# Kernel tuning notes

Measured on AMD Instinct MI355X. Metric: run time of the kernel, lower is better.

The kernel has to match this reference:

```python
import jax, jax.numpy as jnp
import numpy as np

# Model dims (match init_kwargs)
D_MODEL = 2048
H = 16        # query heads
HKV = 4       # kv heads (GQA)
DS = 32       # semantic head dim (compressed)
DG = 32       # geometric head dim (compressed, RoPE'd)
DV = 64       # value head dim
B, T = 2, 4096
MB = 64       # mem_block
LW = 1024     # local_window
ROPE_BASE = 10000.0
NEG_INF = -1e9


def _rope(x, pos, base):
    # x: [B, h, T, d] with d even; standard rotate-half RoPE
    d = x.shape[-1]
    inv_freq = 1.0 / (base ** (jnp.arange(0, d, 2, dtype=jnp.float32) / d))
    ang = pos.astype(jnp.float32)[:, None] * inv_freq          # [T, d/2]
    cos, sin = jnp.cos(ang), jnp.sin(ang)                      # [T, d/2]
    x1, x2 = jnp.split(x, 2, axis=-1)
    return jnp.concatenate([x1 * cos - x2 * sin,
                            x2 * cos + x1 * sin], axis=-1)


def setup_inputs() -> dict:
    key = jax.random.key(0)
    ks = jax.random.split(key, 8)
    w = lambda k, sh: jax.random.normal(k, sh, jnp.float32) * 0.02
    return {
        "x": jax.random.normal(ks[0], (B, T, D_MODEL), jnp.float32),
        "Wq_sem": w(ks[1], (D_MODEL, H * DS)),
        "Wk_sem": w(ks[2], (D_MODEL, HKV * DS)),
        "Wq_geo": w(ks[3], (D_MODEL, H * DG)),
        "Wk_geo": w(ks[4], (D_MODEL, HKV * DG)),
        "Wv": w(ks[5], (D_MODEL, HKV * DV)),
        "Wo": w(ks[6], (H * DV, D_MODEL)),
        "logit_scale": jnp.zeros((H,), jnp.float32),
    }


def reference(x, Wq_sem, Wk_sem, Wq_geo, Wk_geo, Wv, Wo, logit_scale):
    Bq, Tq = x.shape[0], x.shape[1]
    split = lambda y, h, d: y.reshape(Bq, Tq, h, d).transpose(0, 2, 1, 3)
    # Decoupled projections
    q_sem = split(x @ Wq_sem, H, DS)      # [B,H,T,DS]
    k_sem = split(x @ Wk_sem, HKV, DS)    # [B,HKV,T,DS]
    q_geo = split(x @ Wq_geo, H, DG)
    k_geo = split(x @ Wk_geo, HKV, DG)
    v = split(x @ Wv, HKV, DV)            # [B,HKV,T,DV]
    pos = jnp.arange(Tq)
    # RoPE only on the geometric path
    q_geo = _rope(q_geo, pos, ROPE_BASE)
    k_geo = _rope(k_geo, pos, ROPE_BASE)
    # Memory-block summarization: mean-pool remote KV into one token per block
    remote = Tq - LW
    nblk = remote // MB
    pool = lambda a: jnp.concatenate(
        [a[:, :, :remote].reshape(Bq, HKV, nblk, MB, a.shape[-1]).mean(axis=3),
         a[:, :, remote:]], axis=2)
    k_sem2, k_geo2, v2 = pool(k_sem), pool(k_geo), pool(v)  # [B,HKV,K,*], K=nblk+LW
    k_pos = jnp.concatenate([jnp.arange(nblk) * MB + (MB - 1),
                             jnp.arange(remote, Tq)])        # [K]
    # GQA head-group broadcast
    rep = lambda a: jnp.repeat(a, H // HKV, axis=1)
    k_sem2, k_geo2, v2 = rep(k_sem2), rep(k_geo2), rep(v2)   # [B,H,K,*]
    # Decoupled scores: semantic + geometric, each with its own scale
    scores = (jnp.einsum('bhqd,bhkd->bhqk', q_sem, k_sem2) * (1.0 / jnp.sqrt(float(DS)))
              + jnp.einsum('bhqd,bhkd->bhqk', q_geo, k_geo2) * (1.0 / jnp.sqrt(float(DG))))
    # Learned per-head temperature
    scores = scores * jnp.exp(logit_scale)[None, :, None, None]
    # Causal mask over summarized key positions
    mask = k_pos[None, :] <= pos[:, None]                    # [T,K]
    scores = jnp.where(mask[None, None], scores, NEG_INF)
    probs = jax.nn.softmax(scores, axis=-1)
    out = jnp.einsum('bhqk,bhkd->bhqd', probs, v2)           # [B,H,T,DV]
    out = out.transpose(0, 2, 1, 3).reshape(Bq, Tq, H * DV)
    return out @ Wo                                          # [B,T,D_MODEL]
```

## Files before the change

kernel.cpp:

```cpp
#include <hip/hip_runtime.h>
#include <math.h>

#define B_  2
#define T_  4096
#define DM  2048
#define H_  16
#define HKV 4
#define DV_ 64
#define MB_ 64
#define LW_ 1024
#define REMOTE 3072
#define NBLK 48
#define KTOT 1072
#define NTILES 17

typedef __bf16 bf16x8 __attribute__((ext_vector_type(8)));
typedef float  f32x4  __attribute__((ext_vector_type(4)));

__device__ __forceinline__ float bf2f(unsigned short u) {
    unsigned int x = ((unsigned int)u) << 16;
    return __builtin_bit_cast(float, x);
}
__device__ __forceinline__ unsigned short f2bf(float f) {
    unsigned int x = __builtin_bit_cast(unsigned int, f);
    x = x + 0x7fffu + ((x >> 16) & 1u);
    return (unsigned short)(x >> 16);
}

__device__ __forceinline__ void gload16(const void* gsrc, unsigned short* ldst) {
    __builtin_amdgcn_global_load_lds(
        (const __attribute__((address_space(1))) void*)gsrc,
        (__attribute__((address_space(3))) void*)ldst,
        16, 0, 0);
}

__global__ void transpose_all(const float* __restrict__ Wq_sem,
                              const float* __restrict__ Wq_geo,
                              const float* __restrict__ Wk_sem,
                              const float* __restrict__ Wk_geo,
                              const float* __restrict__ Wv,
                              const float* __restrict__ Wo,
                              unsigned short* __restrict__ WcatT,
                              unsigned short* __restrict__ WoT) {
    __shared__ float tile[32][33];
    const int bid = blockIdx.x;
    const float* src; unsigned short* dst; int R, C, tiles_x, lt;
    if (bid < 1024)      { src = Wq_sem; dst = WcatT;                       R = 2048; C = 512;  tiles_x = 16; lt = bid; }
    else if (bid < 2048) { src = Wq_geo; dst = WcatT + (size_t)512  * 2048; R = 2048; C = 512;  tiles_x = 16; lt = bid - 1024; }
    else if (bid < 2304) { src = Wk_sem; dst = WcatT + (size_t)1024 * 2048; R = 2048; C = 128;  tiles_x = 4;  lt = bid - 2048; }
    else if (bid < 2560) { src = Wk_geo; dst = WcatT + (size_t)1152 * 2048; R = 2048; C = 128;  tiles_x = 4;  lt = bid - 2304; }
    else if (bid < 3072) { src = Wv;     dst = WcatT + (size_t)1280 * 2048; R = 2048; C = 256;  tiles_x = 8;  lt = bid - 2560; }
    else                 { src = Wo;     dst = WoT;                         R = 1024; C = 2048; tiles_x = 64; lt = bid - 3072; }
    const int ct = lt % tiles_x, rt = lt / tiles_x;
    const int tx = threadIdx.x, ty = threadIdx.y;
    #pragma unroll
    for (int i = ty; i < 32; i += 8)
        tile[i][tx] = src[(size_t)(rt * 32 + i) * C + ct * 32 + tx];
    __syncthreads();
    #pragma unroll
    for (int i = ty; i < 32; i += 8)
        dst[(size_t)(ct * 32 + i) * R + rt * 32 + tx] = f2bf(tile[tx][i]);
}

__global__ __launch_bounds__(256, 3) void gemmProj(
    const float* __restrict__ Axf0,
    const unsigned short* __restrict__ BT,
    unsigned short* __restrict__ qcat,
    unsigned short* __restrict__ kp,
    unsigned short* __restrict__ vt,
    int K, int nbx)
{
    extern __shared__ __align__(16) unsigned short lds[];

    const int tid = threadIdx.x;
    const int lane = tid & 63, w = tid >> 6;
    const int wr = w >> 1, wc = w & 1;
    const int l15 = lane & 15, lg = lane >> 4;

    const int cpx = gridDim.x >> 3;
    const int swz = (blockIdx.x & 7) * cpx + (blockIdx.x >> 3);
    const int bx = swz % nbx, by = swz / nbx;
    const int row0 = by * 128, col0 = bx * 128;

    const int scol = ((lane & 3) ^ ((lane >> 3) & 3)) * 8;
    const int srA = w * 16 + (lane >> 2);
    const unsigned short* Bg = BT + (size_t)col0 * K;

    const int ar0 = tid >> 2, ar1 = ar0 + 64, ac = tid & 3;
    const int agc0 = (ac ^ ((ar0 >> 1) & 3)) * 8;
    const int agc1 = (ac ^ ((ar1 >> 1) & 3)) * 8;
    const float* Axf = Axf0 + (size_t)row0 * K;

    const int rdsw = (lg ^ ((l15 >> 1) & 3)) * 8;
    const int aoff = (wr * 64 + l15) * 32 + rdsw;
    const int boff = (wc * 64 + l15) * 32 + rdsw;

    const int NT = K >> 5;
    f32x4 acc[4][4] = {};

    auto stageB = [&](int s, int kk) {
        unsigned short* sb = lds + s * 8192 + 4096;
        #pragma unroll
        for (int j = 0; j < 2; j++)
            gload16(Bg + (size_t)(srA + j * 64) * K + kk + scol,
                    sb + (j * 256 + w * 64) * 8);
    };
    auto issueA = [&](float4* ra, int kk) {
        ra[0] = *(const float4*)&Axf[(size_t)ar0 * K + kk + agc0];
        ra[1] = *(const float4*)&Axf[(size_t)ar0 * K + kk + agc0 + 4];
        ra[2] = *(const float4*)&Axf[(size_t)ar1 * K + kk + agc1];
        ra[3] = *(const float4*)&Axf[(size_t)ar1 * K + kk + agc1 + 4];
    };
    auto writeA = [&](int s, const float4* ra) {
        unsigned short* sa = lds + s * 8192;
        bf16x8 v0, v1;
        v0[0] = (__bf16)ra[0].x; v0[1] = (__bf16)ra[0].y;
        v0[2] = (__bf16)ra[0].z; v0[3] = (__bf16)ra[0].w;
        v0[4] = (__bf16)ra[1].x; v0[5] = (__bf16)ra[1].y;
        v0[6] = (__bf16)ra[1].z; v0[7] = (__bf16)ra[1].w;
        v1[0] = (__bf16)ra[2].x; v1[1] = (__bf16)ra[2].y;
        v1[2] = (__bf16)ra[2].z; v1[3] = (__bf16)ra[2].w;
        v1[4] = (__bf16)ra[3].x; v1[5] = (__bf16)ra[3].y;
        v1[6] = (__bf16)ra[3].z; v1[7] = (__bf16)ra[3].w;
        *(uint4*)&sa[ar0 * 32 + ac * 8] = __builtin_bit_cast(uint4, v0);
        *(uint4*)&sa[ar1 * 32 + ac * 8] = __builtin_bit_cast(uint4, v1);
    };
    auto mfmaTile = [&](int rs_) {
        const unsigned short* As_ = lds + rs_ * 8192;
        const unsigned short* Bs_ = As_ + 4096;
        bf16x8 af[4], bfr[4];
        #pragma unroll
        for (int mf = 0; mf < 4; mf++)
            af[mf] = __builtin_bit_cast(bf16x8, *(const uint4*)&As_[aoff + mf * 512]);
        #pragma unroll
        for (int nf = 0; nf < 4; nf++)
            bfr[nf] = __builtin_bit_cast(bf16x8, *(const uint4*)&Bs_[boff + nf * 512]);
        __builtin_amdgcn_s_setprio(1);
        #pragma unroll
        for (int mf = 0; mf < 4; mf++)
            #pragma unroll
            for (int nf = 0; nf < 4; nf++)
                acc[mf][nf] = __builtin_amdgcn_mfma_f32_16x16x32_bf16(
                    af[mf], bfr[nf], acc[mf][nf], 0, 0, 0);
        __builtin_amdgcn_s_setprio(0);
    };

    stageB(0, 0);
    stageB(1, 32);
    __builtin_amdgcn_sched_barrier(0);
    float4 rA[4], rB[4];
    issueA(rA, 0);
    issueA(rB, 32);
    writeA(0, rA);
    asm volatile("s_waitcnt lgkmcnt(0)" ::: "memory");
    __builtin_amdgcn_s_barrier();

    int rs = 0;
    for (int t = 0; t < NT; t += 2) {
        const int s1 = (rs == 2) ? 0 : rs + 1;
        const int s2 = (s1 == 2) ? 0 : s1 + 1;
        if (t + 2 < NT) {
            stageB(s2, (t + 2) << 5);
            __builtin_amdgcn_sched_barrier(0);
            issueA(rA, (t + 2) << 5);
        }
        writeA(s1, rB);
        mfmaTile(rs);
        asm volatile("s_waitcnt lgkmcnt(0)" ::: "memory");
        __builtin_amdgcn_s_barrier();
        if (t + 3 < NT) {
            stageB(rs, (t + 3) << 5);
            __builtin_amdgcn_sched_barrier(0);
            issueA(rB, (t + 3) << 5);
        }
        if (t + 2 < NT) writeA(s2, rA);
        mfmaTile(s1);
        asm volatile("s_waitcnt lgkmcnt(0)" ::: "memory");
        __builtin_amdgcn_s_barrier();
        rs = s2;
    }

    const int cspan = col0 + wc * 64;
    const int tbase = row0 & 4095;
    const int bq = row0 >> 12;

    if ((cspan >= 512 && cspan < 1024) || (cspan >= 1152 && cspan < 1280)) {
        const float invf = exp2f(-(float)l15 * 0.8304820237218406f);
        #pragma unroll
        for (int mf = 0; mf < 4; mf++) {
            #pragma unroll
            for (int r = 0; r < 4; r++) {
                float s, c;
                sincosf((float)(tbase + wr*64 + mf*16 + lg*4 + r) * invf, &s, &c);
                float a0 = acc[mf][0][r], a1 = acc[mf][1][r];
                acc[mf][0][r] = a0 * c - a1 * s;
                acc[mf][1][r] = a1 * c + a0 * s;
                float a2 = acc[mf][2][r], a3 = acc[mf][3][r];
                acc[mf][2][r] = a2 * c - a3 * s;
                acc[mf][3][r] = a3 * c + a2 * s;
            }
        }
    }

    if (cspan < 1024) {
        #pragma unroll
        for (int nf = 0; nf < 4; nf++) {
            int col = cspan + nf * 16 + l15;
            int h = (col < 512) ? (col >> 5) : ((col - 512) >> 5);
            int d = (col < 512) ? (col & 31) : (32 + (col & 31));
            unsigned short* qb =
                qcat + (((size_t)(bq * 16 + h)) * 4096 + tbase) * 64 + d;
            #pragma unroll
            for (int mf = 0; mf < 4; mf++)
                #pragma unroll
                for (int r = 0; r < 4; r++)
                    qb[(size_t)(wr*64 + mf*16 + lg*4 + r) * 64] =
                        f2bf(acc[mf][nf][r]);
        }
    } else if (tbase >= REMOTE) {
        #pragma unroll
        for (int nf = 0; nf < 4; nf++) {
            int col = cspan + nf * 16 + l15;
            #pragma unroll
            for (int mf = 0; mf < 4; mf++)
                #pragma unroll
                for (int r = 0; r < 4; r++) {
                    int key = tbase + wr*64 + mf*16 + lg*4 + r - 3024;
                    unsigned short hv = f2bf(acc[mf][nf][r]);
                    if (col < 1280) {
                        int g, dk;
                        if (col < 1152) { g = (col - 1024) >> 5; dk = col & 31; }
                        else            { g = (col - 1152) >> 5; dk = 32 + (col & 31); }
                        kp[(((size_t)(bq*4 + g)) * KTOT + key) * 64 + dk] = hv;
                    } else {
                        int g = (col - 1280) >> 6, dv = col & 63;
                        vt[(((size_t)(bq*4 + g)) * 64 + dv) * KTOT + key] = hv;
                    }
                }
        }
    } else {
        #pragma unroll
        for (int nf = 0; nf < 4; nf++) {
            float ps = 0.f;
            #pragma unroll
            for (int mf = 0; mf < 4; mf++)
                #pragma unroll
                for (int r = 0; r < 4; r++) ps += acc[mf][nf][r];
            ps += __shfl_xor(ps, 16);
            ps += __shfl_xor(ps, 32);
            if (lane < 16) {
                int col = cspan + nf * 16 + l15;
                int key = (tbase >> 6) + wr;
                unsigned short hv = f2bf(ps * (1.f / 64.f));
                if (col < 1280) {
                    int g, dk;
                    if (col < 1152) { g = (col - 1024) >> 5; dk = col & 31; }
                    else            { g = (col - 1152) >> 5; dk = 32 + (col & 31); }
                    kp[(((size_t)(bq*4 + g)) * KTOT + key) * 64 + dk] = hv;
                } else {
                    int g = (col - 1280) >> 6, dv = col & 63;
                    vt[(((size_t)(bq*4 + g)) * 64 + dv) * KTOT + key] = hv;
                }
            }
        }
    }
}

__global__ __launch_bounds__(256, 2) void gemmWo(
    const unsigned short* __restrict__ A,
    const unsigned short* __restrict__ BT,
    float* __restrict__ outF,
    int N, int K, int nbx)
{
    extern __shared__ __align__(16) unsigned short lds[];

    const int tid = threadIdx.x;
    const int lane = tid & 63, w = tid >> 6;
    const int l15 = lane & 15, lg = lane >> 4;

    const int cpx = gridDim.x >> 3;
    const int swz = (blockIdx.x & 7) * cpx + (blockIdx.x >> 3);
    const int bx = swz % nbx, by = swz / nbx;
    const int row0 = by * 128, col0 = bx * 256;

    const int scol = ((lane & 3) ^ ((lane >> 3) & 3)) * 8;
    const int srA = w * 16 + (lane >> 2);
    const unsigned short* Ag = A  + (size_t)row0 * K;
    const unsigned short* Bg = BT + (size_t)col0 * K;

    const int rdsw = (lg ^ ((l15 >> 1) & 3)) * 8;
    const int aoff = l15 * 32 + rdsw;
    const int boff = (w * 64 + l15) * 32 + rdsw;

    const int NT = K >> 5;
    f32x4 acc[8][4] = {};

    auto stage = [&](int s, int kk) {
        unsigned short* sa = lds + s * 12288;
        unsigned short* sb = sa + 4096;
        #pragma unroll
        for (int j = 0; j < 2; j++)
            gload16(Ag + (size_t)(srA + j * 64) * K + kk + scol,
                    sa + (j * 256 + w * 64) * 8);
        #pragma unroll
        for (int j = 0; j < 4; j++)
            gload16(Bg + (size_t)(srA + j * 64) * K + kk + scol,
                    sb + (j * 256 + w * 64) * 8);
    };

    stage(0, 0);
    stage(1, 32);
    asm volatile("s_waitcnt vmcnt(6)" ::: "memory");

    int rs = 0;
    for (int t = 0; t < NT; ++t) {
        __builtin_amdgcn_s_barrier();
        if (t + 2 < NT) stage(rs == 0 ? 2 : rs - 1, (t + 2) << 5);

        const unsigned short* As_ = lds + rs * 12288;
        const unsigned short* Bs_ = As_ + 4096;
        bf16x8 af[8], bfr[4];
        #pragma unroll
        for (int mf = 0; mf < 8; mf++)
            af[mf] = __builtin_bit_cast(bf16x8, *(const uint4*)&As_[aoff + mf * 512]);
        #pragma unroll
        for (int nf = 0; nf < 4; nf++)
            bfr[nf] = __builtin_bit_cast(bf16x8, *(const uint4*)&Bs_[boff + nf * 512]);

        __builtin_amdgcn_s_setprio(1);
        #pragma unroll
        for (int mf = 0; mf < 8; mf++)
            #pragma unroll
            for (int nf = 0; nf < 4; nf++)
                acc[mf][nf] = __builtin_amdgcn_mfma_f32_16x16x32_bf16(
                                  af[mf], bfr[nf], acc[mf][nf], 0, 0, 0);
        __builtin_amdgcn_s_setprio(0);

        if (t + 2 < NT) asm volatile("s_waitcnt vmcnt(6)" ::: "memory");
        else            asm volatile("s_waitcnt vmcnt(0)" ::: "memory");
        rs = (rs == 2) ? 0 : rs + 1;
    }

    #pragma unroll
    for (int mf = 0; mf < 8; mf++)
        #pragma unroll
        for (int nf = 0; nf < 4; nf++)
            #pragma unroll
            for (int r = 0; r < 4; r++) {
                int row = row0 + mf * 16 + lg * 4 + r;
                int col = col0 + w * 64 + nf * 16 + l15;
                outF[(size_t)row * N + col] = acc[mf][nf][r];
            }
}

__global__ __launch_bounds__(256) void attn_fwd(
    const unsigned short* __restrict__ qcat,
    const unsigned short* __restrict__ kp,
    const unsigned short* __restrict__ vt,
    const float* __restrict__ ls,
    unsigned short* __restrict__ attn_out)
{
    __shared__ unsigned short Pl[4][32][72];

    const int tid = threadIdx.x;
    const int lane = tid & 63, w = tid >> 6;
    const int l15 = lane & 15, lg = lane >> 4;

    const int wid = blockIdx.x * 4 + w;
    const int hb = wid & 31;
    const int iu = wid >> 5;
    int i;
    if (iu < 32)       i = 127 - iu;
    else if (iu == 32) i = 0;
    else if (iu == 33) i = 1;
    else               i = iu - 32;
    const int h = hb & 15, b = hb >> 4, g = h >> 2;
    const int q0 = i * 32;

    int ktmax;
    if (q0 < 64) ktmax = NTILES;
    else {
        int lastkey = q0 + 31 - 3024;
        ktmax = (lastkey < NBLK) ? 1 : (lastkey / 64 + 1);
    }

    const float sc = __expf(ls[h]) * 0.17677669529663687f;

    bf16x8 aq[2][2];
    const unsigned short* qbase = qcat + (((size_t)(b * 16 + h)) * T_ + q0) * 64;
    #pragma unroll
    for (int rf = 0; rf < 2; rf++)
        #pragma unroll
        for (int kh = 0; kh < 2; kh++)
            aq[rf][kh] = __builtin_bit_cast(bf16x8,
                *(const uint4*)(qbase + (size_t)(rf*16 + l15)*64 + kh*32 + lg*8));

    float m[2][4], lrun[2][4];
    #pragma unroll
    for (int rf = 0; rf < 2; rf++)
        #pragma unroll
        for (int r = 0; r < 4; r++) { m[rf][r] = -1e9f; lrun[rf][r] = 0.f; }
    f32x4 oacc[2][4] = {};

    const unsigned short* kbase = kp + ((size_t)(b * 4 + g)) * KTOT * 64;
    const unsigned short* vbase = vt + ((size_t)(b * 4 + g)) * 64 * KTOT;

    for (int kt = 0; kt < ktmax; kt++) {
        const int kb = kt * 64;

        bf16x8 bk[4][2];
        #pragma unroll
        for (int nf = 0; nf < 4; nf++) {
            int krow = kb + nf*16 + l15;
            int krc = krow < KTOT ? krow : KTOT - 1;
            #pragma unroll
            for (int kh = 0; kh < 2; kh++)
                bk[nf][kh] = __builtin_bit_cast(bf16x8,
                    *(const uint4*)(kbase + (size_t)krc * 64 + kh*32 + lg*8));
        }

        f32x4 s[2][4] = {};
        #pragma unroll
        for (int rf = 0; rf < 2; rf++)
            #pragma unroll
            for (int nf = 0; nf < 4; nf++)
                #pragma unroll
                for (int kh = 0; kh < 2; kh++)
                    s[rf][nf] = __builtin_amdgcn_mfma_f32_16x16x32_bf16(
                                    aq[rf][kh], bk[nf][kh], s[rf][nf], 0, 0, 0);

        bf16x8 bv[4][2];
        #pragma unroll
        for (int nfv = 0; nfv < 4; nfv++)
            #pragma unroll
            for (int kh = 0; kh < 2; kh++) {
                int kc = kb + kh*32 + lg*8;
                int kcc = (kc + 8 <= KTOT) ? kc : KTOT - 8;
                bv[nfv][kh] = __builtin_bit_cast(bf16x8,
                    *(const uint4*)(vbase + (size_t)(nfv*16 + l15) * KTOT + kcc));
            }

        #pragma unroll
        for (int rf = 0; rf < 2; rf++) {
            #pragma unroll
            for (int r = 0; r < 4; r++) {
                const int qpos = q0 + rf*16 + lg*4 + r;
                float vals[4];
                float tmax = -INFINITY;
                #pragma unroll
                for (int nf = 0; nf < 4; nf++) {
                    int key = kb + nf*16 + l15;
                    float v = s[rf][nf][r] * sc;
                    int kpos = (key < NBLK) ? key * 64 + 63 : 3024 + key;
                    v = (key < KTOT) ? ((kpos <= qpos) ? v : -1e9f) : -INFINITY;
                    vals[nf] = v;
                    tmax = fmaxf(tmax, v);
                }
                #pragma unroll
                for (int d = 1; d < 16; d <<= 1)
                    tmax = fmaxf(tmax, __shfl_xor(tmax, d));
                float mn = fmaxf(m[rf][r], tmax);
                float scl = __expf(m[rf][r] - mn);
                m[rf][r] = mn;
                float rs = 0.f;
                #pragma unroll
                for (int nf = 0; nf < 4; nf++) {
                    unsigned short pb = f2bf(__expf(vals[nf] - mn));
                    rs += bf2f(pb);
                    Pl[w][rf*16 + lg*4 + r][nf*16 + l15] = pb;
                }
                #pragma unroll
                for (int d = 1; d < 16; d <<= 1)
                    rs += __shfl_xor(rs, d);
                lrun[rf][r] = lrun[rf][r] * scl + rs;
                #pragma unroll
                for (int nfv = 0; nfv < 4; nfv++)
                    oacc[rf][nfv][r] *= scl;
            }
        }

        #pragma unroll
        for (int rf = 0; rf < 2; rf++) {
            bf16x8 pa[2];
            #pragma unroll
            for (int kh = 0; kh < 2; kh++)
                pa[kh] = __builtin_bit_cast(bf16x8,
                    *(const uint4*)&Pl[w][rf*16 + l15][kh*32 + lg*8]);
            #pragma unroll
            for (int nfv = 0; nfv < 4; nfv++)
                #pragma unroll
                for (int kh = 0; kh < 2; kh++)
                    oacc[rf][nfv] = __builtin_amdgcn_mfma_f32_16x16x32_bf16(
                                        pa[kh], bv[nfv][kh], oacc[rf][nfv], 0, 0, 0);
        }
    }

    #pragma unroll
    for (int rf = 0; rf < 2; rf++) {
        #pragma unroll
        for (int r = 0; r < 4; r++) {
            float inv = 1.f / lrun[rf][r];
            int q = q0 + rf*16 + lg*4 + r;
            size_t obase = ((size_t)(b * T_ + q)) * 1024 + h * 64;
            #pragma unroll
            for (int nfv = 0; nfv < 4; nfv++)
                attn_out[obase + nfv*16 + l15] = f2bf(oacc[rf][nfv][r] * inv);
        }
    }
}

extern "C" void kernel_launch(void* const* d_in, const int* in_sizes, int n_in,
                              void* d_out, int out_size, void* d_ws, size_t ws_size,
                              hipStream_t stream) {
    const float* x      = (const float*)d_in[0];
    const float* Wq_sem = (const float*)d_in[1];
    const float* Wk_sem = (const float*)d_in[2];
    const float* Wq_geo = (const float*)d_in[3];
    const float* Wk_geo = (const float*)d_in[4];
    const float* Wv     = (const float*)d_in[5];
    const float* Wo     = (const float*)d_in[6];
    const float* ls     = (const float*)d_in[7];

    char* w = (char*)d_ws;
    auto alloc = [&](size_t bytes) {
        char* p = w;
        w += (bytes + 255) & ~(size_t)255;
        return p;
    };
    unsigned short* WcatT = (unsigned short*)alloc((size_t)1536 * 2048 * 2);
    unsigned short* WoT   = (unsigned short*)alloc((size_t)2048 * 1024 * 2);
    unsigned short* qcat  = (unsigned short*)alloc((size_t)2 * 16 * 4096 * 64 * 2);
    unsigned short* kp    = (unsigned short*)alloc((size_t)2 * 4 * 1072 * 64 * 2);
    unsigned short* vt    = (unsigned short*)alloc((size_t)2 * 4 * 1072 * 64 * 2);
    unsigned short* aout  = (unsigned short*)alloc((size_t)8192 * 1024 * 2);

    hipFuncSetAttribute(reinterpret_cast<const void*>(&gemmProj),
                        hipFuncAttributeMaxDynamicSharedMemorySize, 49152);
    hipFuncSetAttribute(reinterpret_cast<const void*>(&gemmWo),
                        hipFuncAttributeMaxDynamicSharedMemorySize, 73728);

    transpose_all<<<5120, dim3(32, 8), 0, stream>>>(
        Wq_sem, Wq_geo, Wk_sem, Wk_geo, Wv, Wo, WcatT, WoT);

    gemmProj<<<768, 256, 49152, stream>>>(
        x, WcatT, qcat, kp, vt, 2048, 12);

    attn_fwd<<<dim3(1024), 256, 0, stream>>>(qcat, kp, vt, ls, aout);

    gemmWo<<<512, 256, 73728, stream>>>(
        aout, WoT, (float*)d_out, 2048, 1024, 8);
}
```

Baseline: 179.3 us.

## Pre-convert x to bf16 in prep kernel and stream A via LDS DMA

Adds a bf16 conversion of x to the weight-transpose prep kernel, so the projection GEMM loads both A and B tiles with direct global-to-LDS loads. This replaces the old register-staged fp32 A path and its in-loop conversion. The GEMM main loop becomes a simpler single-step triple-buffered pipeline with vmcnt waits. The trade is an extra 32MB write and read of bf16 x (64MB fp32 read moved to prep) in exchange for halved A traffic in a GEMM that re-reads A across 12 column blocks.

```diff
diff --git a/kernel.cpp b/kernel.cpp
--- a/kernel.cpp
+++ b/kernel.cpp
@@ -34,17 +34,30 @@
         16, 0, 0);
 }
 
-__global__ void transpose_all(const float* __restrict__ Wq_sem,
-                              const float* __restrict__ Wq_geo,
-                              const float* __restrict__ Wk_sem,
-                              const float* __restrict__ Wk_geo,
-                              const float* __restrict__ Wv,
-                              const float* __restrict__ Wo,
-                              unsigned short* __restrict__ WcatT,
-                              unsigned short* __restrict__ WoT) {
+__global__ void prep_all(const float* __restrict__ x,
+                         const float* __restrict__ Wq_sem,
+                         const float* __restrict__ Wq_geo,
+                         const float* __restrict__ Wk_sem,
+                         const float* __restrict__ Wk_geo,
+                         const float* __restrict__ Wv,
+                         const float* __restrict__ Wo,
+                         unsigned short* __restrict__ xb,
+                         unsigned short* __restrict__ WcatT,
+                         unsigned short* __restrict__ WoT) {
+    const int bid = blockIdx.x;
+    if (bid >= 5120) {
+        const int base = (bid - 5120) * 256 + threadIdx.x;
+        #pragma unroll
+        for (int it = 0; it < 16; it++) {
+            int i = base + it * 262144;
+            float4 v = ((const float4*)x)[i];
+            ((ushort4*)xb)[i] =
+                make_ushort4(f2bf(v.x), f2bf(v.y), f2bf(v.z), f2bf(v.w));
+        }
+        return;
+    }
     __shared__ float tile[32][33];
-    const int bid = blockIdx.x;
-    const float* src; unsigned short* dst; int R, C, tiles_x, lt;
+    const float* src; unsigned short* dst; int C, R, tiles_x, lt;
     if (bid < 1024)      { src = Wq_sem; dst = WcatT;                       R = 2048; C = 512;  tiles_x = 16; lt = bid; }
     else if (bid < 2048) { src = Wq_geo; dst = WcatT + (size_t)512  * 2048; R = 2048; C = 512;  tiles_x = 16; lt = bid - 1024; }
     else if (bid < 2304) { src = Wk_sem; dst = WcatT + (size_t)1024 * 2048; R = 2048; C = 128;  tiles_x = 4;  lt = bid - 2048; }
@@ -52,7 +65,7 @@
     else if (bid < 3072) { src = Wv;     dst = WcatT + (size_t)1280 * 2048; R = 2048; C = 256;  tiles_x = 8;  lt = bid - 2560; }
     else                 { src = Wo;     dst = WoT;                         R = 1024; C = 2048; tiles_x = 64; lt = bid - 3072; }
     const int ct = lt % tiles_x, rt = lt / tiles_x;
-    const int tx = threadIdx.x, ty = threadIdx.y;
+    const int tx = threadIdx.x & 31, ty = threadIdx.x >> 5;
     #pragma unroll
     for (int i = ty; i < 32; i += 8)
         tile[i][tx] = src[(size_t)(rt * 32 + i) * C + ct * 32 + tx];
@@ -63,7 +76,7 @@
 }
 
 __global__ __launch_bounds__(256, 3) void gemmProj(
-    const float* __restrict__ Axf0,
+    const unsigned short* __restrict__ A,
     const unsigned short* __restrict__ BT,
     unsigned short* __restrict__ qcat,
     unsigned short* __restrict__ kp,
@@ -84,12 +97,8 @@
 
     const int scol = ((lane & 3) ^ ((lane >> 3) & 3)) * 8;
     const int srA = w * 16 + (lane >> 2);
+    const unsigned short* Ag = A  + (size_t)row0 * K;
     const unsigned short* Bg = BT + (size_t)col0 * K;
-
-    const int ar0 = tid >> 2, ar1 = ar0 + 64, ac = tid & 3;
-    const int agc0 = (ac ^ ((ar0 >> 1) & 3)) * 8;
-    const int agc1 = (ac ^ ((ar1 >> 1) & 3)) * 8;
-    const float* Axf = Axf0 + (size_t)row0 * K;
 
     const int rdsw = (lg ^ ((l15 >> 1) & 3)) * 8;
     const int aoff = (wr * 64 + l15) * 32 + rdsw;
@@ -98,35 +107,28 @@
     const int NT = K >> 5;
     f32x4 acc[4][4] = {};
 
-    auto stageB = [&](int s, int kk) {
-        unsigned short* sb = lds + s * 8192 + 4096;
-        #pragma unroll
-        for (int j = 0; j < 2; j++)
+    auto stage = [&](int s, int kk) {
+        unsigned short* sa = lds + s * 8192;
+        unsigned short* sb = sa + 4096;
+        #pragma unroll
+        for (int j = 0; j < 2; j++) {
+            gload16(Ag + (size_t)(srA + j * 64) * K + kk + scol,
+                    sa + (j * 256 + w * 64) * 8);
             gload16(Bg + (size_t)(srA + j * 64) * K + kk + scol,
                     sb + (j * 256 + w * 64) * 8);
+        }
     };
-    auto issueA = [&](float4* ra, int kk) {
-        ra[0] = *(const float4*)&Axf[(size_t)ar0 * K + kk + agc0];
-        ra[1] = *(const float4*)&Axf[(size_t)ar0 * K + kk + agc0 + 4];
-        ra[2] = *(const float4*)&Axf[(size_t)ar1 * K + kk + agc1];
-        ra[3] = *(const float4*)&Axf[(size_t)ar1 * K + kk + agc1 + 4];
-    };
-    auto writeA = [&](int s, const float4* ra) {
-        unsigned short* sa = lds + s * 8192;
-        bf16x8 v0, v1;
-        v0[0] = (__bf16)ra[0].x; v0[1] = (__bf16)ra[0].y;
-        v0[2] = (__bf16)ra[0].z; v0[3] = (__bf16)ra[0].w;
-        v0[4] = (__bf16)ra[1].x; v0[5] = (__bf16)ra[1].y;
-        v0[6] = (__bf16)ra[1].z; v0[7] = (__bf16)ra[1].w;
-        v1[0] = (__bf16)ra[2].x; v1[1] = (__bf16)ra[2].y;
-        v1[2] = (__bf16)ra[2].z; v1[3] = (__bf16)ra[2].w;
-        v1[4] = (__bf16)ra[3].x; v1[5] = (__bf16)ra[3].y;
-        v1[6] = (__bf16)ra[3].z; v1[7] = (__bf16)ra[3].w;
-        *(uint4*)&sa[ar0 * 32 + ac * 8] = __builtin_bit_cast(uint4, v0);
-        *(uint4*)&sa[ar1 * 32 + ac * 8] = __builtin_bit_cast(uint4, v1);
-    };
-    auto mfmaTile = [&](int rs_) {
-        const unsigned short* As_ = lds + rs_ * 8192;
+
+    stage(0, 0);
+    stage(1, 32);
+    asm volatile("s_waitcnt vmcnt(4)" ::: "memory");
+
+    int rs = 0;
+    for (int t = 0; t < NT; ++t) {
+        __builtin_amdgcn_s_barrier();
+        if (t + 2 < NT) stage(rs == 0 ? 2 : rs - 1, (t + 2) << 5);
+
+        const unsigned short* As_ = lds + rs * 8192;
         const unsigned short* Bs_ = As_ + 4096;
         bf16x8 af[4], bfr[4];
         #pragma unroll
@@ -135,49 +137,19 @@
         #pragma unroll
         for (int nf = 0; nf < 4; nf++)
             bfr[nf] = __builtin_bit_cast(bf16x8, *(const uint4*)&Bs_[boff + nf * 512]);
+
         __builtin_amdgcn_s_setprio(1);
         #pragma unroll
         for (int mf = 0; mf < 4; mf++)
             #pragma unroll
             for (int nf = 0; nf < 4; nf++)
                 acc[mf][nf] = __builtin_amdgcn_mfma_f32_16x16x32_bf16(
-                    af[mf], bfr[nf], acc[mf][nf], 0, 0, 0);
+                                  af[mf], bfr[nf], acc[mf][nf], 0, 0, 0);
         __builtin_amdgcn_s_setprio(0);
-    };
-
-    stageB(0, 0);
-    stageB(1, 32);
-    __builtin_amdgcn_sched_barrier(0);
-    float4 rA[4], rB[4];
-    issueA(rA, 0);
-    issueA(rB, 32);
-    writeA(0, rA);
-    asm volatile("s_waitcnt lgkmcnt(0)" ::: "memory");
-    __builtin_amdgcn_s_barrier();
-
-    int rs = 0;
-    for (int t = 0; t < NT; t += 2) {
-        const int s1 = (rs == 2) ? 0 : rs + 1;
-        const int s2 = (s1 == 2) ? 0 : s1 + 1;
-        if (t + 2 < NT) {
-            stageB(s2, (t + 2) << 5);
-            __builtin_amdgcn_sched_barrier(0);
-            issueA(rA, (t + 2) << 5);
-        }
-        writeA(s1, rB);
-        mfmaTile(rs);
-        asm volatile("s_waitcnt lgkmcnt(0)" ::: "memory");
-        __builtin_amdgcn_s_barrier();
-        if (t + 3 < NT) {
-            stageB(rs, (t + 3) << 5);
-            __builtin_amdgcn_sched_barrier(0);
-            issueA(rB, (t + 3) << 5);
-        }
-        if (t + 2 < NT) writeA(s2, rA);
-        mfmaTile(s1);
-        asm volatile("s_waitcnt lgkmcnt(0)" ::: "memory");
-        __builtin_amdgcn_s_barrier();
-        rs = s2;
+
+        if (t + 2 < NT) asm volatile("s_waitcnt vmcnt(4)" ::: "memory");
+        else            asm volatile("s_waitcnt vmcnt(0)" ::: "memory");
+        rs = (rs == 2) ? 0 : rs + 1;
     }
 
     const int cspan = col0 + wc * 64;
@@ -527,6 +499,7 @@
         w += (bytes + 255) & ~(size_t)255;
         return p;
     };
+    unsigned short* xb    = (unsigned short*)alloc((size_t)8192 * 2048 * 2);
     unsigned short* WcatT = (unsigned short*)alloc((size_t)1536 * 2048 * 2);
     unsigned short* WoT   = (unsigned short*)alloc((size_t)2048 * 1024 * 2);
     unsigned short* qcat  = (unsigned short*)alloc((size_t)2 * 16 * 4096 * 64 * 2);
@@ -539,11 +512,11 @@
     hipFuncSetAttribute(reinterpret_cast<const void*>(&gemmWo),
                         hipFuncAttributeMaxDynamicSharedMemorySize, 73728);
 
-    transpose_all<<<5120, dim3(32, 8), 0, stream>>>(
-        Wq_sem, Wq_geo, Wk_sem, Wk_geo, Wv, Wo, WcatT, WoT);
+    prep_all<<<6144, 256, 0, stream>>>(
+        x, Wq_sem, Wq_geo, Wk_sem, Wk_geo, Wv, Wo, xb, WcatT, WoT);
 
     gemmProj<<<768, 256, 49152, stream>>>(
-        x, WcatT, qcat, kp, vt, 2048, 12);
+        xb, WcatT, qcat, kp, vt, 2048, 12);
 
     attn_fwd<<<dim3(1024), 256, 0, stream>>>(qcat, kp, vt, ls, aout);
 
```

New measurement: 187.7 us. 1.05x slower.
